# Kernel tuning notes

Measured on AMD Instinct MI355X. Metric: run time of the kernel, lower is better.

The kernel has to match this reference:

```python
import jax, jax.numpy as jnp
import numpy as np
from jax import lax

BLOCK = 64      # block_size
OVERLAP = 16
NITER = 64      # Niter init kwarg; loop runs min(1000, Niter)
L = 0.24        # diffusion step size
K = 0.03        # exp(logk), logk = log(0.03)
DEPS = 0.1
FFT_STEPS = 10
THRESH = 0.1    # uniform-region variance threshold


def _g(x):
    # g(x) = 1 / (1 + |x^2| / K^2)
    return 1.0 / (1.0 + jnp.abs(x * x) / (K * K))


def _avgpool3(x):
    # F.avg_pool2d(x, 3, stride=1, padding=1) with count_include_pad=True (divide by 9)
    s = lax.reduce_window(x, 0.0, lax.add, (1, 1, 3, 3), (1, 1, 1, 1),
                          [(0, 0), (0, 0), (1, 1), (1, 1)])
    return s / 9.0


def _fft_diffuse_block(block, bcv, bch):
    cv_mean = bcv.mean()
    ch_mean = bch.mean()
    h, w = block.shape[2], block.shape[3]
    ky = jnp.arange(h, dtype=block.dtype)[:, None] * (2.0 * np.pi / h)      # [h,1]
    kx = jnp.arange(w // 2 + 1, dtype=block.dtype)[None, :] * (2.0 * np.pi / w)  # [1,w//2+1]
    op = (1.0 - 2.0 * L * (cv_mean * (1.0 - jnp.cos(ky)) + ch_mean * (1.0 - jnp.cos(kx)))) ** FFT_STEPS
    return jnp.fft.irfft2(jnp.fft.rfft2(block) * op, s=(h, w))


def _forward(guide, initial):
    # depth shift for stability (torch code branches on initial.min() <= deps)
    shift = jnp.where(initial.min() <= DEPS, DEPS, 0.0).astype(initial.dtype)
    depth = initial + shift

    # diffusion coefficients from guide: cv [B,1,H-1,W], ch [B,1,H,W-1]
    cv = _g(jnp.mean(jnp.abs(guide[:, :, 1:, :] - guide[:, :, :-1, :]), axis=1, keepdims=True))
    ch = _g(jnp.mean(jnp.abs(guide[:, :, :, 1:] - guide[:, :, :, :-1]), axis=1, keepdims=True))

    # identify_uniform_regions (local variance via avg pools); original torch code
    # broadcasts shapes (H-1,W) & (H,W-1) which errors -- we crop to common (H-1,W-1)
    cv_var = _avgpool3(cv ** 2) - _avgpool3(cv) ** 2
    ch_var = _avgpool3(ch ** 2) - _avgpool3(ch) ** 2
    uniform = ((cv_var[:, :, :, :-1] < THRESH) & (ch_var[:, :, :-1, :] < THRESH)).astype(depth.dtype)

    B, C, H, W = depth.shape
    step = BLOCK - OVERLAP
    # sequential per-block FFT diffusion with overlap blending (blocks read
    # depth updated by previous blocks, so order matters)
    for b in range(B):
        for y in range(0, H, step):
            for x in range(0, W, step):
                y_end = min(y + BLOCK, H)
                x_end = min(x + BLOCK, W)
                bh, bw = y_end - y, x_end - x
                block = depth[b:b + 1, :, y:y_end, x:x_end]
                bcv = cv[b:b + 1, :, y:y_end - 1, x:x_end]
                bch = ch[b:b + 1, :, y:y_end, x:x_end - 1]
                bun = uniform[b:b + 1, :, y:y_end, x:x_end]  # clips at edges (H-1,W-1)
                cond = bun.mean() > 0.7
                newb = _fft_diffuse_block(block, bcv, bch)
                if y > 0 or x > 0:
                    blend_y = jnp.ones((bh,), depth.dtype)
                    if y > 0:
                        r = jnp.arange(bh)
                        blend_y = jnp.where(r < min(OVERLAP, bh), r.astype(depth.dtype) / OVERLAP, blend_y)
                    blend_x = jnp.ones((bw,), depth.dtype)
                    if x > 0:
                        r = jnp.arange(bw)
                        blend_x = jnp.where(r < min(OVERLAP, bw), r.astype(depth.dtype) / OVERLAP, blend_x)
                    blend = (blend_y[:, None] * blend_x[None, :])[None, None]
                    cand = block * (1.0 - blend) + newb * blend
                else:
                    cand = newb
                region = jnp.where(cond, cand, block)
                depth = depth.at[b:b + 1, :, y:y_end, x:x_end].set(region)

    # explicit anisotropic diffusion stencil, serial data dependence -> lax.scan
    def diffuse_step(I, _):
        dv = I[:, :, 1:, :] - I[:, :, :-1, :]
        dh = I[:, :, :, 1:] - I[:, :, :, :-1]  # computed before vertical update (as in torch)
        tv = L * cv * dv
        I = I.at[:, :, 1:, :].add(-tv).at[:, :, :-1, :].add(tv)
        th = L * ch * dh
        I = I.at[:, :, :, 1:].add(-th).at[:, :, :, :-1].add(th)
        return I, None

    depth, _ = lax.scan(diffuse_step, depth, None, length=min(1000, NITER))
    y_pred = depth - shift
    return y_pred, cv, ch


def setup_inputs() -> dict:
    key = jax.random.key(0)
    k1, k2 = jax.random.split(key)
    guide = jax.random.uniform(k1, (2, 3, 512, 512), dtype=jnp.float32)
    initial = jax.random.uniform(k2, (2, 1, 512, 512), dtype=jnp.float32)
    return {"guide": guide, "initial": initial}


def reference(guide, initial):
    # returns (y_pred, cv, ch) matching {'y_pred':..., 'cv':..., 'ch':...}
    return _forward(guide, initial)
```

## Files before the change

kernel.cpp:

```cpp
#include <hip/hip_runtime.h>
#include <stdint.h>

#define LDIFF 0.24f

constexpr int H = 512, W = 512, NB = 2;
constexpr int HW = H * W;
constexpr int N_D = NB * HW;
constexpr int CVH = 511, CVW = 512;
constexpr int CHH = 512, CHW = 511;
constexpr int N_CV = NB * CVH * CVW;
constexpr int NBLKS = 11;
constexpr int NBT = NB * 121;

__device__ inline float ldc(const float* p) {
    return __hip_atomic_load(p, __ATOMIC_RELAXED, __HIP_MEMORY_SCOPE_AGENT);
}
__device__ inline void stc(float* p, float v) {
    __hip_atomic_store(p, v, __ATOMIC_RELAXED, __HIP_MEMORY_SCOPE_AGENT);
}
__device__ inline int ldci(const int* p) {
    return __hip_atomic_load(p, __ATOMIC_RELAXED, __HIP_MEMORY_SCOPE_AGENT);
}
__device__ inline void stci(int* p, int v) {
    __hip_atomic_store(p, v, __ATOMIC_RELAXED, __HIP_MEMORY_SCOPE_AGENT);
}

__device__ inline float rot_a(float x) {
    return __int_as_float(__builtin_amdgcn_update_dpp(0, __float_as_int(x), 0x134, 0xf, 0xf, false));
}
__device__ inline float rot_b(float x) {
    return __int_as_float(__builtin_amdgcn_update_dpp(0, __float_as_int(x), 0x13c, 0xf, 0xf, false));
}
__device__ inline float sh_a(float x) {
    return __int_as_float(__builtin_amdgcn_update_dpp(0, __float_as_int(x), 0x130, 0xf, 0xf, true));
}
__device__ inline float sh_b(float x) {
    return __int_as_float(__builtin_amdgcn_update_dpp(0, __float_as_int(x), 0x138, 0xf, 0xf, true));
}

#define BSTEP(SRC, DST, LO, HI)                                                   \
    _Pragma("unroll")                                                             \
    for (int m = (LO); m <= (HI); m++) {                                          \
        float hs = rot_a(SRC[m]) + rot_b(SRC[m]);                                 \
        DST[m] = SRC[m] + a * (SRC[m - 1] + SRC[m + 1] - 2.0f * SRC[m])           \
                        + bc * (hs - 2.0f * SRC[m]);                              \
    }

#define CSTEP(SRC, DST, LO, HI)                                                   \
    _Pragma("unroll")                                                             \
    for (int m = (LO); m <= (HI); m++) {                                          \
        float Vm = SRC[m] + LDIFF * cve[m] * (SRC[m + 1] - SRC[m])                \
                          - LDIFF * cve[m - 1] * (SRC[m] - SRC[m - 1]);           \
        float rA = rot_a(Vm), rB = rot_b(Vm);                                     \
        float lf = dirL ? rA : rB, rt = dirL ? rB : rA;                           \
        DST[m] = Vm + LDIFF * che[m] * (rt - Vm) - LDIFF * chle[m] * (Vm - lf);   \
    }

__global__ __launch_bounds__(256) void kall(
    const float* __restrict__ guide, const float* __restrict__ initial,
    float* __restrict__ cv, float* __restrict__ ch,
    float* __restrict__ D, float* __restrict__ T0, float* __restrict__ T1,
    float* __restrict__ ypred, int* __restrict__ sync_)
{
    __shared__ float cvT[73 * 74];
    __shared__ float chT[73 * 74];
    __shared__ float xT[2][4][5][64];
    __shared__ float xB[2][4][5][64];
    __shared__ float red[12];
    __shared__ float prmS[3];

    int* wflag = sync_;
    int* dflag = sync_ + 16384;

    const int blk = blockIdx.x;
    const int i = blk / NBLKS, j = blk % NBLKS;
    const int b = blockIdx.y;
    const int tid = threadIdx.x;
    const int lane = tid & 63, wv = tid >> 6;
    const int r0 = wv * 16;
    const int me = b * 121 + blk;

    const int y0 = i * 48, x0 = j * 48;
    const int y1 = min(y0 + 64, 512), x1 = min(x0 + 64, 512);
    const int bh = y1 - y0, bw = x1 - x0;
    const int yb = y0 - 8, xb = x0 - 8;
    const float kinv = 1.0f / (0.03f * 0.03f);

    const float* gb = guide + (size_t)b * 3 * HW;
    for (int p = tid; p < 73 * 73; p += 256) {
        int rr = p / 73, cc2 = p - rr * 73;
        int y = yb + rr, x = xb + cc2;
        float cvv = 0.0f, chv = 0.0f;
        if (y >= 0 && y < 512 && x >= 0 && x < 512) {
            const float* g = gb + y * W + x;
            float g0 = g[0], g1 = g[HW], g2 = g[2 * HW];
            if (y < 511) {
                float d = (fabsf(g[W] - g0) + fabsf(g[HW + W] - g1) + fabsf(g[2 * HW + W] - g2)) * (1.0f / 3.0f);
                cvv = 1.0f / (1.0f + d * d * kinv);
            }
            if (x < 511) {
                float d = (fabsf(g[1] - g0) + fabsf(g[HW + 1] - g1) + fabsf(g[2 * HW + 1] - g2)) * (1.0f / 3.0f);
                chv = 1.0f / (1.0f + d * d * kinv);
            }
        }
        cvT[rr * 74 + cc2] = cvv;
        chT[rr * 74 + cc2] = chv;
    }
    __syncthreads();

    {
        int rcv = min(y0 + 48, CVH) - y0, ccv = min(x0 + 48, CVW) - x0;
        float* cvo = cv + b * CVH * CVW;
        for (int p = tid; p < rcv * ccv; p += 256) {
            int r = p / ccv, c = p - r * ccv;
            cvo[(y0 + r) * CVW + x0 + c] = cvT[(r + 8) * 74 + c + 8];
        }
        int rch = min(y0 + 48, CHH) - y0, cch = min(x0 + 48, CHW) - x0;
        float* cho = ch + b * CHH * CHW;
        for (int p = tid; p < rch * cch; p += 256) {
            int r = p / cch, c = p - r * cch;
            cho[(y0 + r) * CHW + x0 + c] = chT[(r + 8) * 74 + c + 8];
        }
    }

    float scv = 0.f, sch = 0.f, sun = 0.f;
    {
        int n = (bh - 1) * bw;
        for (int p = tid; p < n; p += 256) { int r = p / bw, c = p - r * bw; scv += cvT[(r + 8) * 74 + c + 8]; }
    }
    {
        int cols = bw - 1, n = bh * cols;
        for (int p = tid; p < n; p += 256) { int r = p / cols, c = p - r * cols; sch += chT[(r + 8) * 74 + c + 8]; }
    }
    const int ur = min(y1, 511) - y0, uc = min(x1, 511) - x0;
    {
        int n = ur * uc;
        for (int p = tid; p < n; p += 256) {
            int r = p / uc, c = p - r * uc;
            float s1 = 0.f, s2 = 0.f, t1 = 0.f, t2 = 0.f;
            #pragma unroll
            for (int dy = 0; dy < 3; dy++)
                #pragma unroll
                for (int dx = 0; dx < 3; dx++) {
                    float v = cvT[(r + 7 + dy) * 74 + c + 7 + dx]; s1 += v; s2 += v * v;
                    float w2 = chT[(r + 7 + dy) * 74 + c + 7 + dx]; t1 += w2; t2 += w2 * w2;
                }
            float m = s1 * (1.0f / 9.0f);
            float vcv = s2 * (1.0f / 9.0f) - m * m;
            m = t1 * (1.0f / 9.0f);
            float vch = t2 * (1.0f / 9.0f) - m * m;
            if (vcv < 0.1f && vch < 0.1f) sun += 1.f;
        }
    }
    #pragma unroll
    for (int m = 1; m < 64; m <<= 1) {
        scv += __shfl_xor(scv, m);
        sch += __shfl_xor(sch, m);
        sun += __shfl_xor(sun, m);
    }
    if (lane == 0) { red[wv * 3] = scv; red[wv * 3 + 1] = sch; red[wv * 3 + 2] = sun; }
    __syncthreads();
    if (tid == 0) {
        float a0 = red[0] + red[3] + red[6] + red[9];
        float a1 = red[1] + red[4] + red[7] + red[10];
        float a2 = red[2] + red[5] + red[8] + red[11];
        prmS[0] = a0 / (float)((bh - 1) * bw);
        prmS[1] = a1 / (float)(bh * (bw - 1));
        prmS[2] = (a2 / (float)(ur * uc) > 0.7f) ? 1.0f : 0.0f;
    }
    __syncthreads();

    int prb = __builtin_amdgcn_update_dpp(0, lane, 0x134, 0xf, 0xf, false);
    const bool dirL = (prb == ((lane + 63) & 63));

    const bool cond = prmS[2] > 0.5f;
    const float a = LDIFF * prmS[0], bc = LDIFF * prmS[1];
    float* Db = D + b * HW;
    const float* ini = initial + b * HW;

    const int mh = bh - 1, mw = bw - 1;
    const int ccw = lane & mw;

    if (!cond) {
        #pragma unroll
        for (int k = 0; k < 16; k++) {
            int r = r0 + k;
            if (r < bh && (i == 0 || r >= 16) && lane < bw && (j == 0 || lane >= 16)) {
                int ad = (y0 + r) * W + x0 + lane;
                stc(&Db[ad], ini[ad]);
            }
        }
        asm volatile("s_waitcnt vmcnt(0)" ::: "memory");
        if (lane == 0) stci(&wflag[me * 64 + wv * 16], 1);
    } else {
        float u[16], orig[16];
        int addr[16]; bool fD[16];
        #pragma unroll
        for (int k = 0; k < 16; k++) {
            int rr = (r0 + k) & mh;
            addr[k] = (y0 + rr) * W + x0 + ccw;
            fD[k] = (i > 0 && rr < 16) || (j > 0 && ccw < 16);
            if (!fD[k]) orig[k] = ini[addr[k]];
        }
        if (wv == 0) {
            bool need = false;
            const int* fp = &wflag[me * 64];
            if (lane < 3) {
                if (j > 0) { need = true; fp = &wflag[(b * 121 + i * NBLKS + j - 1) * 64 + (lane + 1) * 16]; }
            } else if (lane == 3) {
                if (i > 0) { need = true; fp = &wflag[(b * 121 + (i - 1) * NBLKS + j) * 64 + 3 * 16]; }
            } else if (lane == 4) {
                if (i > 0 && j < 10) { need = true; fp = &wflag[(b * 121 + (i - 1) * NBLKS + j + 1) * 64 + 3 * 16]; }
            } else if (lane == 5) {
                if (i > 0 && j > 0) { need = true; fp = &wflag[(b * 121 + (i - 1) * NBLKS + j - 1) * 64 + 3 * 16]; }
            }
            while (true) {
                int v = need ? ldci(fp) : 1;
                if (__ballot(v == 0) == 0) break;
                __builtin_amdgcn_s_sleep(0);
            }
        }
        __syncthreads();
        #pragma unroll
        for (int k = 0; k < 16; k++) if (fD[k]) orig[k] = ldc(&Db[addr[k]]);
        #pragma unroll
        for (int k = 0; k < 16; k++) u[k] = orig[k];

        float wa[26], wb[26];
        #pragma unroll
        for (int g = 0; g < 2; ++g) {
            #pragma unroll
            for (int q = 0; q < 5; q++) {
                xT[g][wv][q][lane] = u[q];
                xB[g][wv][q][lane] = u[11 + q];
            }
            __syncthreads();
            #pragma unroll
            for (int q = 0; q < 5; q++) {
                wa[q]      = xB[g][(wv + 3) & 3][q][lane];
                wa[21 + q] = xT[g][(wv + 1) & 3][q][lane];
            }
            #pragma unroll
            for (int q = 0; q < 16; q++) wa[5 + q] = u[q];
            BSTEP(wa, wb, 1, 24);
            BSTEP(wb, wa, 2, 23);
            BSTEP(wa, wb, 3, 22);
            BSTEP(wb, wa, 4, 21);
            BSTEP(wa, wb, 5, 20);
            #pragma unroll
            for (int q = 0; q < 16; q++) u[q] = wb[5 + q];
        }

        #pragma unroll
        for (int k = 0; k < 16; k++) {
            int r = r0 + k;
            if (r < bh && lane < bw) {
                float byw = (y0 > 0 && r < 16) ? (float)r * (1.0f / 16.0f) : 1.0f;
                float bxw = (x0 > 0 && lane < 16) ? (float)lane * (1.0f / 16.0f) : 1.0f;
                float wgt = byw * bxw;
                stc(&Db[(y0 + r) * W + x0 + lane], orig[k] * (1.0f - wgt) + u[k] * wgt);
            }
        }
        asm volatile("s_waitcnt vmcnt(0)" ::: "memory");
        if (lane == 0) stci(&wflag[me * 64 + wv * 16], 1);
    }
    __syncthreads();

    const int cx = xb + lane;
    const int gxc = min(max(cx, 0), 511);
    int gyA[16];
    #pragma unroll
    for (int k = 0; k < 16; k++) {
        int cy = yb + r0 + k;
        gyA[k] = min(max(cy, 0), 511);
    }
    float cve[24], che[24], chle[24];
    #pragma unroll
    for (int m = 0; m < 24; m++) {
        int rr = r0 + m - 4;
        bool ok = (rr >= 0);
        cve[m] = ok ? cvT[rr * 74 + lane] : 0.0f;
        che[m] = ok ? chT[rr * 74 + lane] : 0.0f;
        chle[m] = dirL ? sh_a(che[m]) : sh_b(che[m]);
    }

    float* Tb0 = T0 + b * HW;
    float* Tb1 = T1 + b * HW;
    float* ypb = ypred + b * HW;
    const bool cok = (lane >= 8 && lane < 56 && xb + lane < 512);

    for (int t = 1; t <= 8; t++) {
        if (wv == 0) {
            bool need = false;
            const int* fp = &wflag[me * 64];
            int thr = 1;
            if (t == 1) {
                if (lane < 36) {
                    int nb = lane >> 2;
                    int di = nb / 3 - 1, dj = nb % 3 - 1;
                    int ni = i + di, nj = j + dj;
                    if ((di | dj) != 0 && ni >= 0 && ni < NBLKS && nj >= 0 && nj < NBLKS) {
                        need = true;
                        fp = &wflag[(b * 121 + ni * NBLKS + nj) * 64 + (lane & 3) * 16];
                    }
                }
            } else {
                thr = t - 1;
                if (lane < 9) {
                    int di = lane / 3 - 1, dj = lane % 3 - 1;
                    int ni = i + di, nj = j + dj;
                    if ((di | dj) != 0 && ni >= 0 && ni < NBLKS && nj >= 0 && nj < NBLKS) {
                        need = true;
                        fp = &dflag[(b * 121 + ni * NBLKS + nj) * 16];
                    }
                }
            }
            while (true) {
                int v = need ? ldci(fp) : 0x7fffffff;
                if (__ballot(v < thr) == 0) break;
                __builtin_amdgcn_s_sleep(8);
            }
        }
        __syncthreads();
        const float* src = (t == 1) ? Db : (((t - 1) & 1) ? Tb1 : Tb0);
        float u[16];
        #pragma unroll
        for (int k = 0; k < 16; k++) u[k] = ldc(&src[gyA[k] * W + gxc]);

        #pragma unroll
        for (int g = 0; g < 2; ++g) {
            #pragma unroll
            for (int q = 0; q < 4; q++) {
                xT[g][wv][q][lane] = u[q];
                xB[g][wv][q][lane] = u[12 + q];
            }
            __syncthreads();
            float wa[24], wb[24];
            #pragma unroll
            for (int q = 0; q < 4; q++) {
                wa[q]      = (wv > 0) ? xB[g][wv - 1][q][lane] : u[0];
                wa[20 + q] = (wv < 3) ? xT[g][wv + 1][q][lane] : u[15];
            }
            #pragma unroll
            for (int q = 0; q < 16; q++) wa[4 + q] = u[q];
            CSTEP(wa, wb, 1, 22);
            CSTEP(wb, wa, 2, 21);
            CSTEP(wa, wb, 3, 20);
            CSTEP(wb, wa, 4, 19);
            #pragma unroll
            for (int q = 0; q < 16; q++) u[q] = wa[4 + q];
        }

        if (t < 8) {
            float* dst = (t & 1) ? Tb1 : Tb0;
            if (cok) {
                #pragma unroll
                for (int k = 0; k < 16; k++) {
                    int r = r0 + k;
                    if (r >= 8 && r < 56) {
                        int y = yb + r;
                        if (y < 512) stc(&dst[y * W + xb + lane], u[k]);
                    }
                }
            }
            asm volatile("s_waitcnt vmcnt(0)" ::: "memory");
            __syncthreads();
            if (tid == 0) stci(&dflag[me * 16], t);
        } else {
            if (cok) {
                #pragma unroll
                for (int k = 0; k < 16; k++) {
                    int r = r0 + k;
                    if (r >= 8 && r < 56) {
                        int y = yb + r;
                        if (y < 512) ypb[y * W + xb + lane] = u[k];
                    }
                }
            }
        }
    }
}

extern "C" void kernel_launch(void* const* d_in, const int* in_sizes, int n_in,
                              void* d_out, int out_size, void* d_ws, size_t ws_size,
                              hipStream_t stream) {
    const float* guide   = (const float*)d_in[0];
    const float* initial = (const float*)d_in[1];
    float* y_pred = (float*)d_out;
    float* cv = y_pred + N_D;
    float* ch = cv + N_CV;

    uint8_t* w = (uint8_t*)d_ws;
    int* sync_ = (int*)w;
    float* D  = (float*)(w + 131072);
    float* T0 = (float*)(w + 131072 + (size_t)N_D * 4);
    float* T1 = (float*)(w + 131072 + (size_t)2 * N_D * 4);

    (void)hipMemsetAsync(sync_, 0, 131072, stream);
    kall<<<dim3(121, NB), 256, 0, stream>>>(guide, initial, cv, ch, D, T0, T1, y_pred, sync_);
}
```

Before: 323.0 us.

## Split block flags into early/late halves, per-wave waits, and keep core values in registers

```diff
diff --git a/kernel.cpp b/kernel.cpp
--- a/kernel.cpp
+++ b/kernel.cpp
@@ -191,7 +191,10 @@
             }
         }
         asm volatile("s_waitcnt vmcnt(0)" ::: "memory");
-        if (lane == 0) stci(&wflag[me * 64 + wv * 16], 1);
+        if (lane == 0) {
+            stci(&wflag[me * 64 + wv * 16], 1);
+            stci(&wflag[me * 64 + wv * 16 + 8], 1);
+        }
     } else {
         float u[16], orig[16];
         int addr[16]; bool fD[16];
@@ -202,17 +205,19 @@
             fD[k] = (i > 0 && rr < 16) || (j > 0 && ccw < 16);
             if (!fD[k]) orig[k] = ini[addr[k]];
         }
-        if (wv == 0) {
+        {
+            const int Lw = (r0 & mh) >> 4;
+            const bool needU = (i > 0) && ((r0 & mh) < 16);
             bool need = false;
             const int* fp = &wflag[me * 64];
-            if (lane < 3) {
-                if (j > 0) { need = true; fp = &wflag[(b * 121 + i * NBLKS + j - 1) * 64 + (lane + 1) * 16]; }
+            if (lane == 0) {
+                if (j > 0) { need = true; fp = &wflag[(me - 1) * 64 + Lw * 16]; }
+            } else if (lane == 1) {
+                if (needU) { need = true; fp = &wflag[(me - NBLKS) * 64 + 3 * 16]; }
+            } else if (lane == 2) {
+                if (needU && j < 10) { need = true; fp = &wflag[(me - NBLKS + 1) * 64 + 3 * 16]; }
             } else if (lane == 3) {
-                if (i > 0) { need = true; fp = &wflag[(b * 121 + (i - 1) * NBLKS + j) * 64 + 3 * 16]; }
-            } else if (lane == 4) {
-                if (i > 0 && j < 10) { need = true; fp = &wflag[(b * 121 + (i - 1) * NBLKS + j + 1) * 64 + 3 * 16]; }
-            } else if (lane == 5) {
-                if (i > 0 && j > 0) { need = true; fp = &wflag[(b * 121 + (i - 1) * NBLKS + j - 1) * 64 + 3 * 16]; }
+                if (needU && j > 0) { need = true; fp = &wflag[(me - NBLKS - 1) * 64 + 3 * 16]; }
             }
             while (true) {
                 int v = need ? ldci(fp) : 1;
@@ -220,7 +225,6 @@
                 __builtin_amdgcn_s_sleep(0);
             }
         }
-        __syncthreads();
         #pragma unroll
         for (int k = 0; k < 16; k++) if (fD[k]) orig[k] = ldc(&Db[addr[k]]);
         #pragma unroll
@@ -254,15 +258,29 @@
         #pragma unroll
         for (int k = 0; k < 16; k++) {
             int r = r0 + k;
-            if (r < bh && lane < bw) {
-                float byw = (y0 > 0 && r < 16) ? (float)r * (1.0f / 16.0f) : 1.0f;
-                float bxw = (x0 > 0 && lane < 16) ? (float)lane * (1.0f / 16.0f) : 1.0f;
-                float wgt = byw * bxw;
-                stc(&Db[(y0 + r) * W + x0 + lane], orig[k] * (1.0f - wgt) + u[k] * wgt);
-            }
+            float byw = (y0 > 0 && r < 16) ? (float)r * (1.0f / 16.0f) : 1.0f;
+            float bxw = (x0 > 0 && lane < 16) ? (float)lane * (1.0f / 16.0f) : 1.0f;
+            float wgt = byw * bxw;
+            u[k] = orig[k] * (1.0f - wgt) + u[k] * wgt;
+        }
+        #pragma unroll
+        for (int k = 0; k < 16; k++) {
+            int r = r0 + k;
+            bool in = (r < bh && lane < bw);
+            bool sc = (bw == 64 && lane >= 48) || (r >= 48);
+            if (in && sc) stc(&Db[(y0 + r) * W + x0 + lane], u[k]);
         }
         asm volatile("s_waitcnt vmcnt(0)" ::: "memory");
         if (lane == 0) stci(&wflag[me * 64 + wv * 16], 1);
+        #pragma unroll
+        for (int k = 0; k < 16; k++) {
+            int r = r0 + k;
+            bool in = (r < bh && lane < bw);
+            bool sc = (bw == 64 && lane >= 48) || (r >= 48);
+            if (in && !sc) stc(&Db[(y0 + r) * W + x0 + lane], u[k]);
+        }
+        asm volatile("s_waitcnt vmcnt(0)" ::: "memory");
+        if (lane == 0) stci(&wflag[me * 64 + wv * 16 + 8], 1);
     }
     __syncthreads();
 
@@ -287,8 +305,19 @@
     float* Tb0 = T0 + b * HW;
     float* Tb1 = T1 + b * HW;
     float* ypb = ypred + b * HW;
-    const bool cok = (lane >= 8 && lane < 56 && xb + lane < 512);
-
+
+    const int coreh = min(48, 512 - y0), corew = min(48, 512 - x0);
+    const bool laneC = (lane >= 8) && (lane < 8 + corew);
+    bool ownc[16], ringk[16];
+    #pragma unroll
+    for (int k = 0; k < 16; k++) {
+        int wr = r0 + k;
+        ownc[k] = laneC && (wr >= 8) && (wr < 8 + coreh);
+        int cr = wr - 8, cl = lane - 8;
+        ringk[k] = ownc[k] && (cr < 8 || cr >= coreh - 8 || cl < 8 || cl >= corew - 8);
+    }
+
+    float u[16];
     for (int t = 1; t <= 8; t++) {
         if (wv == 0) {
             bool need = false;
@@ -301,7 +330,7 @@
                     int ni = i + di, nj = j + dj;
                     if ((di | dj) != 0 && ni >= 0 && ni < NBLKS && nj >= 0 && nj < NBLKS) {
                         need = true;
-                        fp = &wflag[(b * 121 + ni * NBLKS + nj) * 64 + (lane & 3) * 16];
+                        fp = &wflag[(b * 121 + ni * NBLKS + nj) * 64 + (lane & 3) * 16 + 8];
                     }
                 }
             } else {
@@ -323,9 +352,13 @@
         }
         __syncthreads();
         const float* src = (t == 1) ? Db : (((t - 1) & 1) ? Tb1 : Tb0);
-        float u[16];
-        #pragma unroll
-        for (int k = 0; k < 16; k++) u[k] = ldc(&src[gyA[k] * W + gxc]);
+        if (t == 1) {
+            #pragma unroll
+            for (int k = 0; k < 16; k++) u[k] = ldc(&src[gyA[k] * W + gxc]);
+        } else {
+            #pragma unroll
+            for (int k = 0; k < 16; k++) if (!ownc[k]) u[k] = ldc(&src[gyA[k] * W + gxc]);
+        }
 
         #pragma unroll
         for (int g = 0; g < 2; ++g) {
@@ -353,29 +386,17 @@
 
         if (t < 8) {
             float* dst = (t & 1) ? Tb1 : Tb0;
-            if (cok) {
-                #pragma unroll
-                for (int k = 0; k < 16; k++) {
-                    int r = r0 + k;
-                    if (r >= 8 && r < 56) {
-                        int y = yb + r;
-                        if (y < 512) stc(&dst[y * W + xb + lane], u[k]);
-                    }
-                }
+            #pragma unroll
+            for (int k = 0; k < 16; k++) {
+                if (ringk[k]) stc(&dst[(yb + r0 + k) * W + xb + lane], u[k]);
             }
             asm volatile("s_waitcnt vmcnt(0)" ::: "memory");
             __syncthreads();
             if (tid == 0) stci(&dflag[me * 16], t);
         } else {
-            if (cok) {
-                #pragma unroll
-                for (int k = 0; k < 16; k++) {
-                    int r = r0 + k;
-                    if (r >= 8 && r < 56) {
-                        int y = yb + r;
-                        if (y < 512) ypb[y * W + xb + lane] = u[k];
-                    }
-                }
+            #pragma unroll
+            for (int k = 0; k < 16; k++) {
+                if (ownc[k]) ypb[(yb + r0 + k) * W + xb + lane] = u[k];
             }
         }
     }
```

New measurement: 307.0 us. -4.9%, faster.
